# Kernel optimization log

Hardware: AMD Instinct MI355X
Metric: run time of the kernel (lower is better)

The kernel has to match this reference:

```python
import jax, jax.numpy as jnp
import numpy as np

N_NODES = 100000
H = 256
E = 500000

def setup_inputs() -> dict:
    key = jax.random.key(0)
    ks = jax.random.split(key, 7)
    z_src = jax.random.normal(ks[0], (N_NODES, H), dtype=jnp.float32)
    z_dst = jax.random.normal(ks[1], (N_NODES, H), dtype=jnp.float32)
    edge_label_index = jax.random.randint(ks[2], (2, E), 0, N_NODES, dtype=jnp.int64)
    # Linear params, scaled like torch default init (~1/sqrt(fan_in))
    w1 = jax.random.normal(ks[3], (H, 2 * H), dtype=jnp.float32) * (1.0 / np.sqrt(2 * H))
    b1 = jax.random.normal(ks[4], (H,), dtype=jnp.float32) * (1.0 / np.sqrt(2 * H))
    w2 = jax.random.normal(ks[5], (1, H), dtype=jnp.float32) * (1.0 / np.sqrt(H))
    b2 = jax.random.normal(ks[6], (1,), dtype=jnp.float32) * (1.0 / np.sqrt(H))
    return {"z_src": z_src, "z_dst": z_dst, "edge_label_index": edge_label_index,
            "w1": w1, "b1": b1, "w2": w2, "b2": b2}

def reference(z_src, z_dst, edge_label_index, w1, b1, w2, b2):
    row, col = edge_label_index[0], edge_label_index[1]
    # gather edge endpoint features and concat -> [E, 2H]
    z = jnp.concatenate([z_src[row], z_dst[col]], axis=-1)
    z = jax.nn.relu(jnp.einsum('eh,oh->eo', z, w1) + b1)  # [E, H]
    z = jnp.einsum('eh,oh->eo', z, w2) + b2               # [E, 1]
    return jax.nn.sigmoid(z).reshape(-1)
```

## Files before the change

kernel.cpp:

```cpp
#include <hip/hip_runtime.h>
#include <hip/hip_bf16.h>

#define E_TOT 500000
#define N_NODES 100000
#define NUNITS_H 3125
#define SRD 128

typedef __attribute__((ext_vector_type(16))) float f32x16;
typedef __attribute__((ext_vector_type(8))) short short8;
typedef __attribute__((ext_vector_type(4))) float f32x4;

__device__ __forceinline__ unsigned short f2bf(float f) {
  union { float f; unsigned u; } x; x.f = f;
  unsigned r = x.u + 0x7fffu + ((x.u >> 16) & 1u);
  return (unsigned short)(r >> 16);
}

__device__ __forceinline__ float bf2f(unsigned short s) {
  union { unsigned u; float f; } x; x.u = ((unsigned)s) << 16;
  return x.f;
}

__device__ __forceinline__ short cvt1(float f) {
  __hip_bfloat16 h = __float2bfloat16(f);
  union { __hip_bfloat16 h; short s; } u; u.h = h;
  return u.s;
}

__device__ __forceinline__ void gl_lds16(const void* g, void* l) {
  __builtin_amdgcn_global_load_lds(
      (const __attribute__((address_space(1))) void*)g,
      (__attribute__((address_space(3))) void*)l, 16, 0, 0);
}

__global__ void k_repack_w1h(const float* __restrict__ w1,
                             unsigned short* __restrict__ w1r2) {
  int o = blockIdx.x * 256 + threadIdx.x;
  int half = o >> 16;
  int kb = (o >> 11) & 31;
  int n = (o >> 3) & 255;
  int j = o & 7;
  w1r2[o] = f2bf(w1[n * 512 + half * 256 + kb * 8 + j]);
}

__global__ __launch_bounds__(512, 1) void k_node_gemm(
    const float* __restrict__ zsrc, const float* __restrict__ zdst,
    const unsigned short* __restrict__ w1r2, const float* __restrict__ b1,
    unsigned short* __restrict__ Uo, unsigned short* __restrict__ Vo) {
  __shared__ __align__(16) char smem[114688];
  unsigned short* Ct = (unsigned short*)(smem + 98304);

  const int half = blockIdx.x >> 7;
  const int bh = blockIdx.x & 127;
  const float* Z = half ? zdst : zsrc;
  unsigned short* O = half ? Vo : Uo;

  const unsigned tid = threadIdx.x;
  const unsigned l = tid & 63u;
  const unsigned wv = tid >> 6;
  const unsigned l31 = l & 31u;
  const unsigned hi = l >> 5;
  const unsigned xr = (l31 & 7u) << 4;

  short8 brg[16];
  {
    const unsigned short* bb = w1r2 + (unsigned)half * 65536u;
#pragma unroll
    for (int k = 0; k < 16; ++k) {
      unsigned ks = (unsigned)k * 2u + hi;
      brg[k] = *(const short8*)(bb + (ks * 256u + wv * 32u + l31) * 8u);
      asm volatile("" : "+v"(brg[k]));
    }
  }

  const float bi = half ? 0.f : b1[wv * 32u + l31];

#define STAGE(uu, bf)                                                     \
  {                                                                       \
    int uc_ = (uu); if (uc_ >= NUNITS_H) uc_ = NUNITS_H - 1;              \
    const char* src_ = (const char*)(Z + (long)uc_ * 32 * 256);           \
    char* dst_ = smem + (unsigned)(bf)*32768u;                            \
    _Pragma("unroll") for (int q = 0; q < 4; ++q) {                       \
      unsigned row_ = wv * 4u + (unsigned)q;                              \
      unsigned off_ = row_ * 1024u;                                       \
      unsigned so_ = off_ + ((l * 16u) ^ ((row_ & 7u) << 4));             \
      gl_lds16(src_ + so_, dst_ + off_);                                  \
    }                                                                     \
  }

  int u = bh;
  STAGE(u, 0);
  STAGE(u + SRD, 1);
  asm volatile("s_waitcnt vmcnt(4)" ::: "memory");
  __builtin_amdgcn_s_barrier();

  int bufc = 0;
  for (; u < NUNITS_H; u += SRD) {
    int bn = bufc + 2; if (bn >= 3) bn -= 3;
    STAGE(u + 2 * SRD, bn);
    __builtin_amdgcn_sched_barrier(0);
    asm volatile("s_waitcnt vmcnt(8)" ::: "memory");
    __builtin_amdgcn_s_barrier();

    const char* Ab = smem + (unsigned)bufc * 32768u;
    f32x16 acc = {0.f, 0.f, 0.f, 0.f, 0.f, 0.f, 0.f, 0.f,
                  0.f, 0.f, 0.f, 0.f, 0.f, 0.f, 0.f, 0.f};
#pragma unroll
    for (int kk = 0; kk < 16; ++kk) {
      unsigned c0 = (unsigned)kk * 64u + hi * 32u;
      f32x4 a0 = *(const f32x4*)(Ab + l31 * 1024u + (c0 ^ xr));
      f32x4 a1 = *(const f32x4*)(Ab + l31 * 1024u + ((c0 + 16u) ^ xr));
      short8 af;
      af[0] = cvt1(a0.x); af[1] = cvt1(a0.y);
      af[2] = cvt1(a0.z); af[3] = cvt1(a0.w);
      af[4] = cvt1(a1.x); af[5] = cvt1(a1.y);
      af[6] = cvt1(a1.z); af[7] = cvt1(a1.w);
      acc = __builtin_amdgcn_mfma_f32_32x32x16_bf16(af, brg[kk], acc, 0, 0, 0);
    }

#pragma unroll
    for (int r = 0; r < 16; ++r) {
      unsigned row32 = (unsigned)((r & 3) + 8 * (r >> 2)) + 4u * hi;
      Ct[row32 * 256u + wv * 32u + l31] = f2bf(acc[r] + bi);
    }
    asm volatile("s_waitcnt lgkmcnt(0)" ::: "memory");
    __builtin_amdgcn_s_barrier();

    {
      const long gbase = (long)u * 32 * 256;
#pragma unroll
      for (int p = 0; p < 2; ++p) {
        unsigned s = (unsigned)p * 512u + tid;
        unsigned row = s >> 5;
        unsigned seg = s & 31u;
        short8 vv = *(const short8*)&Ct[row * 256u + seg * 8u];
        *(short8*)(O + gbase + row * 256u + seg * 8u) = vv;
      }
    }
    bufc = (bufc == 2) ? 0 : bufc + 1;
  }
#undef STAGE
}

#define EK_ITER 16
__global__ __launch_bounds__(256, 6) void k_edge(
    const unsigned short* __restrict__ U, const unsigned short* __restrict__ V,
    const int* __restrict__ eli, const float* __restrict__ w2,
    const float* __restrict__ b2, float* __restrict__ out) {
  const int tid = threadIdx.x;
  const int g = tid >> 4;
  const int j = tid & 15;
  float w2v[16];
#pragma unroll
  for (int q = 0; q < 8; ++q) {
    w2v[q] = w2[8 * j + q];
    w2v[8 + q] = w2[128 + 8 * j + q];
  }
  const float b2v = b2[0];
  const long base = (long)blockIdx.x * (16 * EK_ITER) + g;

#define CLAMP_E(k) \
  (((base + 16 * (k)) < E_TOT) ? (base + 16 * (k)) : (long)(E_TOT - 1))

  long eP = CLAMP_E(0);
  int rA = eli[eP], cA = eli[E_TOT + eP];
  long eQ = CLAMP_E(1);
  int rB = eli[eQ], cB = eli[E_TOT + eQ];
  short8 uA0 = *(const short8*)(U + (long)rA * 256 + 8 * j);
  short8 uA1 = *(const short8*)(U + (long)rA * 256 + 128 + 8 * j);
  short8 vA0 = *(const short8*)(V + (long)cA * 256 + 8 * j);
  short8 vA1 = *(const short8*)(V + (long)cA * 256 + 128 + 8 * j);
  short8 uB0, uB1, vB0, vB1;

#pragma unroll
  for (int it2 = 0; it2 < EK_ITER / 2; ++it2) {
    {
      long eN = CLAMP_E(2 * it2 + 2);
      int rN = eli[eN], cN = eli[E_TOT + eN];
      uB0 = *(const short8*)(U + (long)rB * 256 + 8 * j);
      uB1 = *(const short8*)(U + (long)rB * 256 + 128 + 8 * j);
      vB0 = *(const short8*)(V + (long)cB * 256 + 8 * j);
      vB1 = *(const short8*)(V + (long)cB * 256 + 128 + 8 * j);
      rB = rN; cB = cN;
      float p = 0.f;
#pragma unroll
      for (int q = 0; q < 8; ++q) {
        float a0 = bf2f((unsigned short)uA0[q]) + bf2f((unsigned short)vA0[q]);
        float a1 = bf2f((unsigned short)uA1[q]) + bf2f((unsigned short)vA1[q]);
        p = fmaf(fmaxf(a0, 0.f), w2v[q], p);
        p = fmaf(fmaxf(a1, 0.f), w2v[8 + q], p);
      }
      p += __shfl_xor(p, 1);
      p += __shfl_xor(p, 2);
      p += __shfl_xor(p, 4);
      p += __shfl_xor(p, 8);
      long e = base + 16 * (2 * it2);
      if (j == 0 && e < E_TOT) out[e] = 1.f / (1.f + __expf(-(p + b2v)));
    }
    {
      long eN = CLAMP_E(2 * it2 + 3);
      int rN = eli[eN], cN = eli[E_TOT + eN];
      uA0 = *(const short8*)(U + (long)rB * 256 + 8 * j);
      uA1 = *(const short8*)(U + (long)rB * 256 + 128 + 8 * j);
      vA0 = *(const short8*)(V + (long)cB * 256 + 8 * j);
      vA1 = *(const short8*)(V + (long)cB * 256 + 128 + 8 * j);
      rB = rN; cB = cN;
      float p = 0.f;
#pragma unroll
      for (int q = 0; q < 8; ++q) {
        float a0 = bf2f((unsigned short)uB0[q]) + bf2f((unsigned short)vB0[q]);
        float a1 = bf2f((unsigned short)uB1[q]) + bf2f((unsigned short)vB1[q]);
        p = fmaf(fmaxf(a0, 0.f), w2v[q], p);
        p = fmaf(fmaxf(a1, 0.f), w2v[8 + q], p);
      }
      p += __shfl_xor(p, 1);
      p += __shfl_xor(p, 2);
      p += __shfl_xor(p, 4);
      p += __shfl_xor(p, 8);
      long e = base + 16 * (2 * it2 + 1);
      if (j == 0 && e < E_TOT) out[e] = 1.f / (1.f + __expf(-(p + b2v)));
    }
  }
#undef CLAMP_E
}

extern "C" void kernel_launch(void* const* d_in, const int* in_sizes, int n_in,
                              void* d_out, int out_size, void* d_ws,
                              size_t ws_size, hipStream_t stream) {
  const float* zsrc = (const float*)d_in[0];
  const float* zdst = (const float*)d_in[1];
  const int* eli = (const int*)d_in[2];
  const float* w1 = (const float*)d_in[3];
  const float* b1 = (const float*)d_in[4];
  const float* w2 = (const float*)d_in[5];
  const float* b2 = (const float*)d_in[6];
  float* out = (float*)d_out;

  const size_t uv_bytes = (size_t)N_NODES * 256 * 2;
  unsigned short* U = (unsigned short*)d_ws;
  unsigned short* V = (unsigned short*)((char*)d_ws + uv_bytes);
  unsigned short* w1r2 = (unsigned short*)((char*)d_ws + 2 * uv_bytes);

  k_repack_w1h<<<512, 256, 0, stream>>>(w1, w1r2);
  k_node_gemm<<<256, 512, 0, stream>>>(zsrc, zdst, w1r2, b1, U, V);
  int nbe = (E_TOT + 16 * EK_ITER - 1) / (16 * EK_ITER);
  k_edge<<<nbe, 256, 0, stream>>>(U, V, eli, w2, b2, out);
}
```

Baseline: 138.1 us.

## Process 64-row node tiles with double-buffering instead of 32-row triple-buffering

The node GEMM now handles 64 rows per unit, issuing two MFMA chains that reuse the same register-resident weight fragments. Staging changes from triple to double buffering with 64KB buffers, and the last partial tile is handled with row clamping and masked stores. The aim is to halve loop iterations and barrier overhead per row and to raise MFMA work per sync. In exchange, prefetch depth drops from two stages to one, so less load latency is hidden, and LDS use grows to 160KB.

```diff
diff --git a/kernel.cpp b/kernel.cpp
--- a/kernel.cpp
+++ b/kernel.cpp
@@ -3,7 +3,7 @@
 
 #define E_TOT 500000
 #define N_NODES 100000
-#define NUNITS_H 3125
+#define NUNITS_H 1563
 #define SRD 128
 
 typedef __attribute__((ext_vector_type(16))) float f32x16;
@@ -47,8 +47,8 @@
     const float* __restrict__ zsrc, const float* __restrict__ zdst,
     const unsigned short* __restrict__ w1r2, const float* __restrict__ b1,
     unsigned short* __restrict__ Uo, unsigned short* __restrict__ Vo) {
-  __shared__ __align__(16) char smem[114688];
-  unsigned short* Ct = (unsigned short*)(smem + 98304);
+  __shared__ __align__(16) char smem[163840];
+  unsigned short* Ct = (unsigned short*)(smem + 131072);
 
   const int half = blockIdx.x >> 7;
   const int bh = blockIdx.x & 127;
@@ -78,33 +78,33 @@
 #define STAGE(uu, bf)                                                     \
   {                                                                       \
     int uc_ = (uu); if (uc_ >= NUNITS_H) uc_ = NUNITS_H - 1;              \
-    const char* src_ = (const char*)(Z + (long)uc_ * 32 * 256);           \
-    char* dst_ = smem + (unsigned)(bf)*32768u;                            \
-    _Pragma("unroll") for (int q = 0; q < 4; ++q) {                       \
-      unsigned row_ = wv * 4u + (unsigned)q;                              \
-      unsigned off_ = row_ * 1024u;                                       \
-      unsigned so_ = off_ + ((l * 16u) ^ ((row_ & 7u) << 4));             \
-      gl_lds16(src_ + so_, dst_ + off_);                                  \
+    char* dst_ = smem + (unsigned)(bf)*65536u;                            \
+    _Pragma("unroll") for (int q = 0; q < 8; ++q) {                       \
+      unsigned row_ = wv * 8u + (unsigned)q;                              \
+      long grow_ = (long)uc_ * 64 + row_;                                 \
+      if (grow_ > N_NODES - 1) grow_ = N_NODES - 1;                       \
+      const char* src_ = (const char*)(Z + grow_ * 256);                  \
+      gl_lds16(src_ + (((l * 16u) ^ ((row_ & 7u) << 4))),                 \
+               dst_ + row_ * 1024u);                                      \
     }                                                                     \
   }
 
   int u = bh;
   STAGE(u, 0);
-  STAGE(u + SRD, 1);
-  asm volatile("s_waitcnt vmcnt(4)" ::: "memory");
+  asm volatile("s_waitcnt vmcnt(0)" ::: "memory");
   __builtin_amdgcn_s_barrier();
 
-  int bufc = 0;
+  int cur = 0;
   for (; u < NUNITS_H; u += SRD) {
-    int bn = bufc + 2; if (bn >= 3) bn -= 3;
-    STAGE(u + 2 * SRD, bn);
+    STAGE(u + SRD, cur ^ 1);
     __builtin_amdgcn_sched_barrier(0);
     asm volatile("s_waitcnt vmcnt(8)" ::: "memory");
     __builtin_amdgcn_s_barrier();
 
-    const char* Ab = smem + (unsigned)bufc * 32768u;
-    f32x16 acc = {0.f, 0.f, 0.f, 0.f, 0.f, 0.f, 0.f, 0.f,
-                  0.f, 0.f, 0.f, 0.f, 0.f, 0.f, 0.f, 0.f};
+    const char* Ab = smem + (unsigned)cur * 65536u;
+    f32x16 acc0 = {0.f, 0.f, 0.f, 0.f, 0.f, 0.f, 0.f, 0.f,
+                   0.f, 0.f, 0.f, 0.f, 0.f, 0.f, 0.f, 0.f};
+    f32x16 acc1 = acc0;
 #pragma unroll
     for (int kk = 0; kk < 16; ++kk) {
       unsigned c0 = (unsigned)kk * 64u + hi * 32u;
@@ -115,29 +115,39 @@
       af[2] = cvt1(a0.z); af[3] = cvt1(a0.w);
       af[4] = cvt1(a1.x); af[5] = cvt1(a1.y);
       af[6] = cvt1(a1.z); af[7] = cvt1(a1.w);
-      acc = __builtin_amdgcn_mfma_f32_32x32x16_bf16(af, brg[kk], acc, 0, 0, 0);
+      acc0 = __builtin_amdgcn_mfma_f32_32x32x16_bf16(af, brg[kk], acc0, 0, 0, 0);
+      f32x4 b0 = *(const f32x4*)(Ab + (32u + l31) * 1024u + (c0 ^ xr));
+      f32x4 b1v = *(const f32x4*)(Ab + (32u + l31) * 1024u + ((c0 + 16u) ^ xr));
+      af[0] = cvt1(b0.x); af[1] = cvt1(b0.y);
+      af[2] = cvt1(b0.z); af[3] = cvt1(b0.w);
+      af[4] = cvt1(b1v.x); af[5] = cvt1(b1v.y);
+      af[6] = cvt1(b1v.z); af[7] = cvt1(b1v.w);
+      acc1 = __builtin_amdgcn_mfma_f32_32x32x16_bf16(af, brg[kk], acc1, 0, 0, 0);
     }
 
 #pragma unroll
     for (int r = 0; r < 16; ++r) {
       unsigned row32 = (unsigned)((r & 3) + 8 * (r >> 2)) + 4u * hi;
-      Ct[row32 * 256u + wv * 32u + l31] = f2bf(acc[r] + bi);
+      Ct[row32 * 256u + wv * 32u + l31] = f2bf(acc0[r] + bi);
+      Ct[(32u + row32) * 256u + wv * 32u + l31] = f2bf(acc1[r] + bi);
     }
     asm volatile("s_waitcnt lgkmcnt(0)" ::: "memory");
     __builtin_amdgcn_s_barrier();
 
     {
-      const long gbase = (long)u * 32 * 256;
-#pragma unroll
-      for (int p = 0; p < 2; ++p) {
+      const long gr0 = (long)u * 64;
+#pragma unroll
+      for (int p = 0; p < 4; ++p) {
         unsigned s = (unsigned)p * 512u + tid;
         unsigned row = s >> 5;
         unsigned seg = s & 31u;
-        short8 vv = *(const short8*)&Ct[row * 256u + seg * 8u];
-        *(short8*)(O + gbase + row * 256u + seg * 8u) = vv;
+        if (gr0 + row < N_NODES) {
+          short8 vv = *(const short8*)&Ct[row * 256u + seg * 8u];
+          *(short8*)(O + (gr0 + row) * 256 + seg * 8u) = vv;
+        }
       }
     }
-    bufc = (bufc == 2) ? 0 : bufc + 1;
+    cur ^= 1;
   }
 #undef STAGE
 }
```

Result: no change. 140.4 us (+1.7%).
